# Kernel tuning notes

Measured on AMD Instinct MI355X. Metric: run time of the kernel, lower is better.

The kernel has to match this reference:

```python
import jax, jax.numpy as jnp
import numpy as np

B, TQ, TK = 4, 128, 512
DQ = DK = DV = H = 1024


def setup_inputs() -> dict:
    key = jax.random.key(0)
    ks = jax.random.split(key, 7)
    s = 0.05  # keep tanh out of saturation
    return {
        "query": jax.random.normal(ks[0], (B, TQ, DQ), dtype=jnp.float32),
        "key": jax.random.normal(ks[1], (B, TK, DK), dtype=jnp.float32),
        "value": jax.random.normal(ks[2], (B, TK, DV), dtype=jnp.float32),
        "Wq": jax.random.normal(ks[3], (DQ, H), dtype=jnp.float32) * s,
        "bq": jax.random.normal(ks[4], (H,), dtype=jnp.float32) * s,
        "Wk": jax.random.normal(ks[5], (DK, H), dtype=jnp.float32) * s,
        "v": jax.random.normal(ks[6], (H,), dtype=jnp.float32) * s,
    }


def reference(query, key, value, Wq, bq, Wk, v):
    # additive (Bahdanau) attention
    wq = jnp.einsum("bqd,dh->bqh", query, Wq) + bq      # [B,Tq,H]
    uh = jnp.einsum("bkd,dh->bkh", key, Wk)             # [B,Tk,H]
    # broadcast add -> [B,Tq,Tk,H], tanh, project to scalar score
    scores = jnp.einsum("bqkh,h->bqk",
                        jnp.tanh(wq[:, :, None, :] + uh[:, None, :, :]), v)
    attn = jax.nn.softmax(scores, axis=-1)              # [B,Tq,Tk]
    h = jnp.einsum("bqk,bkv->bqv", attn, value)         # [B,Tq,Dv]
    return h, attn
```

## Files before the change

### kernel.cpp

```cpp
#include <hip/hip_runtime.h>
#include <hip/hip_bf16.h>

typedef float f32x4 __attribute__((ext_vector_type(4)));
typedef float f32x2 __attribute__((ext_vector_type(2)));
typedef short s16x8 __attribute__((ext_vector_type(8)));
typedef short s16x4 __attribute__((ext_vector_type(4)));

#define NB  4
#define NTQ 128
#define NTK 512
#define NH  1024
#define ECLAMP 3.0e4f

__device__ __forceinline__ unsigned short f2bf(float x) {
    unsigned u = __builtin_bit_cast(unsigned, x);
    u += 0x7FFFu + ((u >> 16) & 1u);
    return (unsigned short)(u >> 16);
}

#define K2E  2.8853900817779268f

#define GLD16(gp, lp) __builtin_amdgcn_global_load_lds( \
    (const __attribute__((address_space(1))) unsigned int*)(gp), \
    (__attribute__((address_space(3))) unsigned int*)(lp), 16, 0, 0)

__global__ __launch_bounds__(256) void prep_kernel(
    const float* __restrict__ Q, const float* __restrict__ K,
    const float* __restrict__ Wq, const float* __restrict__ Wk,
    const float* __restrict__ value,
    short* __restrict__ Qb, short* __restrict__ Kb,
    short* __restrict__ WqT, short* __restrict__ WkT, short* __restrict__ valT)
{
    const int t = threadIdx.x, bx = blockIdx.x;
    if (bx < 640) {
        const float* src; short* dst; size_t base;
        if (bx < 128) { src = Q; dst = Qb; base = (size_t)bx * 4096; }
        else          { src = K; dst = Kb; base = (size_t)(bx - 128) * 4096; }
        #pragma unroll
        for (int i = 0; i < 4; ++i) {
            const size_t off = base + (size_t)(i * 256 + t) * 4;
            const float4 vv = *(const float4*)(src + off);
            s16x4 o = { (short)f2bf(vv.x), (short)f2bf(vv.y),
                        (short)f2bf(vv.z), (short)f2bf(vv.w) };
            *(s16x4*)(dst + off) = o;
        }
        return;
    }
    __shared__ float tile[64][65];
    const int i = bx - 640;
    const float* src; short* dst; int Cs, Rs, r0, c0;
    if (i < 256)      { src = Wq; dst = WqT; Cs = 1024; Rs = 1024; r0 = (i >> 4) * 64; c0 = (i & 15) * 64; }
    else if (i < 512) { const int j = i - 256; src = Wk; dst = WkT; Cs = 1024; Rs = 1024; r0 = (j >> 4) * 64; c0 = (j & 15) * 64; }
    else {
        const int j = i - 512, b = j >> 7, ti = j & 127;
        src = value + (size_t)b * 512 * 1024; dst = valT + (size_t)b * 1024 * 512;
        Cs = 1024; Rs = 512; r0 = (ti >> 4) * 64; c0 = (ti & 15) * 64;
    }
    {
        const int c = (t & 15) * 4;
        #pragma unroll
        for (int it = 0; it < 4; ++it) {
            const int r = (t >> 4) + it * 16;
            const float4 vv = *(const float4*)(src + (size_t)(r0 + r) * Cs + c0 + c);
            tile[r][c + 0] = vv.x; tile[r][c + 1] = vv.y;
            tile[r][c + 2] = vv.z; tile[r][c + 3] = vv.w;
        }
    }
    __syncthreads();
    {
        const int r = (t & 15) * 4;
        #pragma unroll
        for (int it = 0; it < 4; ++it) {
            const int c = (t >> 4) + it * 16;
            s16x4 o = { (short)f2bf(tile[r + 0][c]), (short)f2bf(tile[r + 1][c]),
                        (short)f2bf(tile[r + 2][c]), (short)f2bf(tile[r + 3][c]) };
            *(s16x4*)(dst + (size_t)(c0 + c) * Rs + r0 + r) = o;
        }
    }
}

__global__ __launch_bounds__(256) void mm_kernel(
    const short* __restrict__ Qb, const short* __restrict__ Kb,
    const short* __restrict__ WqT, const short* __restrict__ WkT,
    const float* __restrict__ bq,
    float* __restrict__ Ea_out, unsigned short* __restrict__ EbT)
{
    __shared__ short ldsA[2][128][64];
    __shared__ short ldsB[2][64][64];
    const int t = threadIdx.x;
    const int bx0 = blockIdx.x;
    const int bx = (bx0 & 7) * 40 + (bx0 >> 3);
    const bool g1 = bx < 64;
    const short *A, *B; int m0, n0;
    if (g1) { A = Qb; B = WqT; m0 = (bx >> 4) * 128; n0 = (bx & 15) * 64; }
    else    { const int i = bx - 64; A = Kb; B = WkT; m0 = (i >> 4) * 128; n0 = (i & 15) * 64; }
    A += (size_t)m0 * 1024; B += (size_t)n0 * 1024;

    f32x4 acc[4][2];
    #pragma unroll
    for (int i = 0; i < 4; ++i)
        #pragma unroll
        for (int j = 0; j < 2; ++j) acc[i][j] = f32x4{0.f, 0.f, 0.f, 0.f};

    const int lane = t & 63, wid = t >> 6;
    const int wr = wid >> 1, wc = wid & 1;
    const int fr = lane & 15, fko = (lane >> 4) * 16;

    #define STAGE_MM(buf, k0) do {                                              \
        _Pragma("unroll")                                                       \
        for (int it = 0; it < 4; ++it) {                                        \
            const int idx = it * 256 + t;                                       \
            const int row = idx >> 3, c16 = idx & 7;                            \
            const int sc = c16 ^ (row & 7);                                     \
            GLD16(A + (size_t)row * 1024 + (k0) + sc * 8,                       \
                  &ldsA[buf][0][0] + idx * 8);                                  \
        }                                                                       \
        _Pragma("unroll")                                                       \
        for (int it = 0; it < 2; ++it) {                                        \
            const int idx = it * 256 + t;                                       \
            const int row = idx >> 3, c16 = idx & 7;                            \
            const int sc = c16 ^ (row & 7);                                     \
            GLD16(B + (size_t)row * 1024 + (k0) + sc * 8,                       \
                  &ldsB[buf][0][0] + idx * 8);                                  \
        }                                                                       \
    } while (0)

    #define COMPUTE_MM(buf) do {                                                \
        _Pragma("unroll")                                                       \
        for (int kk = 0; kk < 2; ++kk) {                                        \
            s16x8 af[4], bfv[2];                                                \
            _Pragma("unroll")                                                   \
            for (int i = 0; i < 4; ++i) {                                       \
                const int rowA = wr * 64 + i * 16 + fr;                         \
                int offA = rowA * 128 + kk * 64 + fko; offA ^= (rowA & 7) << 4; \
                af[i] = *(const s16x8*)((const char*)&ldsA[buf][0][0] + offA);  \
            }                                                                   \
            _Pragma("unroll")                                                   \
            for (int ni = 0; ni < 2; ++ni) {                                    \
                const int rowB = wc * 32 + ni * 16 + fr;                        \
                int offB = rowB * 128 + kk * 64 + fko; offB ^= (rowB & 7) << 4; \
                bfv[ni] = *(const s16x8*)((const char*)&ldsB[buf][0][0] + offB);\
            }                                                                   \
            _Pragma("unroll")                                                   \
            for (int mi = 0; mi < 4; ++mi)                                      \
                _Pragma("unroll")                                               \
                for (int ni = 0; ni < 2; ++ni)                                  \
                    acc[mi][ni] = __builtin_amdgcn_mfma_f32_16x16x32_bf16(      \
                                      af[mi], bfv[ni], acc[mi][ni], 0, 0, 0);   \
        }                                                                       \
    } while (0)

    STAGE_MM(0, 0);
    __syncthreads();
    int cur = 0;
    for (int s = 0; s < 15; ++s) {
        STAGE_MM(cur ^ 1, (s + 1) * 64);
        COMPUTE_MM(cur);
        __syncthreads();
        cur ^= 1;
    }
    COMPUTE_MM(cur);

    const int row0 = (lane >> 4) * 4;
    if (g1) {
        #pragma unroll
        for (int ni = 0; ni < 2; ++ni) {
            const int n = n0 + wc * 32 + ni * 16 + fr;
            const float bias = bq[n];
            #pragma unroll
            for (int mi = 0; mi < 4; ++mi) {
                const int m = m0 + wr * 64 + mi * 16 + row0;
                #pragma unroll
                for (int j = 0; j < 4; ++j)
                    Ea_out[(size_t)(m + j) * 1024 + n] =
                        fminf(__builtin_amdgcn_exp2f(K2E * (acc[mi][ni][j] + bias)), ECLAMP);
            }
        }
    } else {
        #pragma unroll
        for (int mi = 0; mi < 4; ++mi) {
            const int m = m0 + wr * 64 + mi * 16 + row0;
            const int b = m >> 9, kk = m & 511;
            #pragma unroll
            for (int ni = 0; ni < 2; ++ni) {
                const int n = n0 + wc * 32 + ni * 16 + fr;
                s16x4 ev;
                #pragma unroll
                for (int j = 0; j < 4; ++j)
                    ev[j] = (short)f2bf(fminf(__builtin_amdgcn_exp2f(K2E * acc[mi][ni][j]), ECLAMP));
                *(s16x4*)&EbT[((size_t)b * 1024 + n) * 512 + kk] = ev;
            }
        }
    }
    #undef STAGE_MM
    #undef COMPUTE_MM
}

__global__ __launch_bounds__(1024, 8) void scores_z(
    const unsigned short* __restrict__ EbT, const float* __restrict__ Ea,
    const float* __restrict__ v, float* __restrict__ zout)
{
    __shared__ float4 s_eav[1024];
    __shared__ float  s_part[16][2][256];
    const int t = threadIdx.x, bx = blockIdx.x;
    const int combo = bx & 7;
    const int b  = combo >> 1, kh = combo & 1;
    const int q2 = bx >> 3;
    const int bq0 = b * 128 + q2 * 2;
    const int kq = t & 63;
    const int hs = t >> 6;

    s_eav[t] = make_float4(Ea[(size_t)(bq0 + 0) * 1024 + t],
                           Ea[(size_t)(bq0 + 1) * 1024 + t],
                           v[t], 0.f);
    __syncthreads();

    const int h0 = hs * 64;
    const uint2* up = (const uint2*)(EbT + ((size_t)(b * 1024 + h0)) * 512
                                     + kh * 256 + kq * 4);
    float a00 = 0.f, a01 = 0.f, a02 = 0.f, a03 = 0.f;
    float a10 = 0.f, a11 = 0.f, a12 = 0.f, a13 = 0.f;
    #pragma unroll 2
    for (int hg = 0; hg < 16; ++hg) {
        const int hb = hg * 4;
        const uint2 r0 = up[(size_t)(hb + 0) * 128];
        const uint2 r1 = up[(size_t)(hb + 1) * 128];
        const uint2 r2 = up[(size_t)(hb + 2) * 128];
        const uint2 r3 = up[(size_t)(hb + 3) * 128];
        const float4 ev0 = s_eav[h0 + hb + 0];
        const float4 ev1 = s_eav[h0 + hb + 1];
        const float4 ev2 = s_eav[h0 + hb + 2];
        const float4 ev3 = s_eav[h0 + hb + 3];
        float eb0[4], eb1[4], eb2[4], eb3[4];
        eb0[0] = __builtin_bit_cast(float, r0.x << 16);
        eb0[1] = __builtin_bit_cast(float, r0.x & 0xFFFF0000u);
        eb0[2] = __builtin_bit_cast(float, r0.y << 16);
        eb0[3] = __builtin_bit_cast(float, r0.y & 0xFFFF0000u);
        eb1[0] = __builtin_bit_cast(float, r1.x << 16);
        eb1[1] = __builtin_bit_cast(float, r1.x & 0xFFFF0000u);
        eb1[2] = __builtin_bit_cast(float, r1.y << 16);
        eb1[3] = __builtin_bit_cast(float, r1.y & 0xFFFF0000u);
        eb2[0] = __builtin_bit_cast(float, r2.x << 16);
        eb2[1] = __builtin_bit_cast(float, r2.x & 0xFFFF0000u);
        eb2[2] = __builtin_bit_cast(float, r2.y << 16);
        eb2[3] = __builtin_bit_cast(float, r2.y & 0xFFFF0000u);
        eb3[0] = __builtin_bit_cast(float, r3.x << 16);
        eb3[1] = __builtin_bit_cast(float, r3.x & 0xFFFF0000u);
        eb3[2] = __builtin_bit_cast(float, r3.y << 16);
        eb3[3] = __builtin_bit_cast(float, r3.y & 0xFFFF0000u);

        #define GRP4(accv, ea0, ea1, ea2, ea3, kk) do {                         \
            const float u0 = __builtin_fmaf(ea0, eb0[kk], 1.0f);                \
            const float u1 = __builtin_fmaf(ea1, eb1[kk], 1.0f);                \
            const float u2 = __builtin_fmaf(ea2, eb2[kk], 1.0f);                \
            const float u3 = __builtin_fmaf(ea3, eb3[kk], 1.0f);                \
            const float d01 = u0 * u1, d23 = u2 * u3;                           \
            float n01 = ev0.z * u1; n01 = __builtin_fmaf(ev1.z, u0, n01);       \
            float n23 = ev2.z * u3; n23 = __builtin_fmaf(ev3.z, u2, n23);       \
            float n = n01 * d23; n = __builtin_fmaf(n23, d01, n);               \
            const float r = __builtin_amdgcn_rcpf(d01 * d23);                   \
            accv = __builtin_fmaf(n, r, accv);                                  \
        } while (0)

        GRP4(a00, ev0.x, ev1.x, ev2.x, ev3.x, 0);
        GRP4(a01, ev0.x, ev1.x, ev2.x, ev3.x, 1);
        GRP4(a02, ev0.x, ev1.x, ev2.x, ev3.x, 2);
        GRP4(a03, ev0.x, ev1.x, ev2.x, ev3.x, 3);
        GRP4(a10, ev0.y, ev1.y, ev2.y, ev3.y, 0);
        GRP4(a11, ev0.y, ev1.y, ev2.y, ev3.y, 1);
        GRP4(a12, ev0.y, ev1.y, ev2.y, ev3.y, 2);
        GRP4(a13, ev0.y, ev1.y, ev2.y, ev3.y, 3);
        #undef GRP4
    }
    *(f32x4*)&s_part[hs][0][kq * 4] = f32x4{a00, a01, a02, a03};
    *(f32x4*)&s_part[hs][1][kq * 4] = f32x4{a10, a11, a12, a13};
    __syncthreads();

    if (t < 512) {
        const int kk = t & 255, qq = t >> 8;
        float z = 0.f;
        #pragma unroll
        for (int j = 0; j < 16; ++j) z += s_part[j][qq][kk];
        zout[(size_t)(bq0 + qq) * 512 + kh * 256 + kk] = -2.0f * z;
    }
}

__global__ __launch_bounds__(512) void softmax_kernel(
    const float* __restrict__ zin, float* __restrict__ attn_out,
    short* __restrict__ attnb)
{
    __shared__ float s_red[16];
    const int t = threadIdx.x, bqi = blockIdx.x;
    const float z = zin[(size_t)bqi * 512 + t];
    const int lane = t & 63, wid = t >> 6;

    float m = z;
    #pragma unroll
    for (int off = 32; off > 0; off >>= 1)
        m = fmaxf(m, __shfl_xor(m, off, 64));
    if (lane == 0) s_red[wid] = m;
    __syncthreads();
    float mx = s_red[0];
    #pragma unroll
    for (int w = 1; w < 8; ++w) mx = fmaxf(mx, s_red[w]);
    const float p = __expf(z - mx);
    __syncthreads();

    float sl = p;
    #pragma unroll
    for (int off = 32; off > 0; off >>= 1)
        sl += __shfl_xor(sl, off, 64);
    if (lane == 0) s_red[wid] = sl;
    __syncthreads();
    float s = 0.f;
    #pragma unroll
    for (int w = 0; w < 8; ++w) s += s_red[w];

    const float a = p * (1.0f / s);
    attn_out[(size_t)bqi * 512 + t] = a;
    attnb[(size_t)bqi * 512 + t] = (short)f2bf(a);
}

__global__ __launch_bounds__(256) void pv_gemm(
    const short* __restrict__ attnb, const short* __restrict__ valT,
    float* __restrict__ outh)
{
    __shared__ short ldsA[2][128][64];
    __shared__ short ldsB[2][64][64];
    const int t = threadIdx.x, bx = blockIdx.x;
    const int b = bx >> 4, nt = bx & 15;
    const int n0 = nt * 64;
    const short* A = attnb + (size_t)b * 128 * 512;
    const short* B = valT + (size_t)b * 1024 * 512 + (size_t)n0 * 512;

    f32x4 acc[4][2];
    #pragma unroll
    for (int i = 0; i < 4; ++i)
        #pragma unroll
        for (int j = 0; j < 2; ++j) acc[i][j] = f32x4{0.f, 0.f, 0.f, 0.f};

    const int lane = t & 63, wid = t >> 6;
    const int wr = wid >> 1, wc = wid & 1;
    const int fr = lane & 15, fko = (lane >> 4) * 16;

    #define STAGE_PV(buf, k0) do {                                              \
        _Pragma("unroll")                                                       \
        for (int it = 0; it < 4; ++it) {                                        \
            const int idx = it * 256 + t;                                       \
            const int row = idx >> 3, c16 = idx & 7;                            \
            const int sc = c16 ^ (row & 7);                                     \
            GLD16(A + (size_t)row * 512 + (k0) + sc * 8,                        \
                  &ldsA[buf][0][0] + idx * 8);                                  \
        }                                                                       \
        _Pragma("unroll")                                                       \
        for (int it = 0; it < 2; ++it) {                                        \
            const int idx = it * 256 + t;                                       \
            const int row = idx >> 3, c16 = idx & 7;                            \
            const int sc = c16 ^ (row & 7);                                     \
            GLD16(B + (size_t)row * 512 + (k0) + sc * 8,                        \
                  &ldsB[buf][0][0] + idx * 8);                                  \
        }                                                                       \
    } while (0)

    #define COMPUTE_PV(buf) do {                                                \
        _Pragma("unroll")                                                       \
        for (int kk = 0; kk < 2; ++kk) {                                        \
            s16x8 af[4], bfv[2];                                                \
            _Pragma("unroll")                                                   \
            for (int i = 0; i < 4; ++i) {                                       \
                const int rowA = wr * 64 + i * 16 + fr;                         \
                int offA = rowA * 128 + kk * 64 + fko; offA ^= (rowA & 7) << 4; \
                af[i] = *(const s16x8*)((const char*)&ldsA[buf][0][0] + offA);  \
            }                                                                   \
            _Pragma("unroll")                                                   \
            for (int ni = 0; ni < 2; ++ni) {                                    \
                const int rowB = wc * 32 + ni * 16 + fr;                        \
                int offB = rowB * 128 + kk * 64 + fko; offB ^= (rowB & 7) << 4; \
                bfv[ni] = *(const s16x8*)((const char*)&ldsB[buf][0][0] + offB);\
            }                                                                   \
            _Pragma("unroll")                                                   \
            for (int mi = 0; mi < 4; ++mi)                                      \
                _Pragma("unroll")                                               \
                for (int ni = 0; ni < 2; ++ni)                                  \
                    acc[mi][ni] = __builtin_amdgcn_mfma_f32_16x16x32_bf16(      \
                                      af[mi], bfv[ni], acc[mi][ni], 0, 0, 0);   \
        }                                                                       \
    } while (0)

    STAGE_PV(0, 0);
    __syncthreads();
    int cur = 0;
    for (int s = 0; s < 7; ++s) {
        STAGE_PV(cur ^ 1, (s + 1) * 64);
        COMPUTE_PV(cur);
        __syncthreads();
        cur ^= 1;
    }
    COMPUTE_PV(cur);

    const int row0 = (lane >> 4) * 4;
    #pragma unroll
    for (int ni = 0; ni < 2; ++ni) {
        const int n = n0 + wc * 32 + ni * 16 + fr;
        #pragma unroll
        for (int mi = 0; mi < 4; ++mi) {
            const int m = wr * 64 + mi * 16 + row0;
            #pragma unroll
            for (int j = 0; j < 4; ++j)
                outh[(size_t)(b * 128 + m + j) * 1024 + n] = acc[mi][ni][j];
        }
    }
    #undef STAGE_PV
    #undef COMPUTE_PV
}

extern "C" void kernel_launch(void* const* d_in, const int* in_sizes, int n_in,
                              void* d_out, int out_size, void* d_ws, size_t ws_size,
                              hipStream_t stream)
{
    const float* query = (const float*)d_in[0];
    const float* key   = (const float*)d_in[1];
    const float* value = (const float*)d_in[2];
    const float* Wq    = (const float*)d_in[3];
    const float* bq    = (const float*)d_in[4];
    const float* Wk    = (const float*)d_in[5];
    const float* v     = (const float*)d_in[6];
    float* out = (float*)d_out;

    char* w = (char*)d_ws;
    float*          ws_Ea  = (float*)w;
    unsigned short* ws_EbT = (unsigned short*)(w + (2u << 20));
    short* Qb     = (short*)(w + (6u << 20));
    short* Kb     = (short*)(w + (7u << 20));
    short* WqT    = (short*)(w + (11u << 20));
    short* WkT    = (short*)(w + (13u << 20));
    short* valT   = (short*)(w + (15u << 20));
    short* attnb  = (short*)(w + (19u << 20));
    float* zbuf   = (float*)(w + (20u << 20));

    float* out_h    = out;
    float* out_attn = out + (size_t)NB * NTQ * NH;

    prep_kernel   <<<dim3(1664), dim3(256),  0, stream>>>(query, key, Wq, Wk, value,
                                                          Qb, Kb, WqT, WkT, valT);
    mm_kernel     <<<dim3(320),  dim3(256),  0, stream>>>(Qb, Kb, WqT, WkT, bq, ws_Ea, ws_EbT);
    scores_z      <<<dim3(512),  dim3(1024), 0, stream>>>(ws_EbT, ws_Ea, v, zbuf);
    softmax_kernel<<<dim3(512),  dim3(512),  0, stream>>>(zbuf, out_attn, attnb);
    pv_gemm       <<<dim3(64),   dim3(256),  0, stream>>>(attnb, valT, out_h);
}
```

Measured before the change: 66.76 us.

## Fuse score reduction with softmax into one kernel covering full key range

```diff
diff --git a/kernel.cpp b/kernel.cpp
--- a/kernel.cpp
+++ b/kernel.cpp
@@ -196,32 +196,33 @@
     #undef COMPUTE_MM
 }
 
-__global__ __launch_bounds__(1024, 8) void scores_z(
+__global__ __launch_bounds__(1024, 4) void scores_softmax(
     const unsigned short* __restrict__ EbT, const float* __restrict__ Ea,
-    const float* __restrict__ v, float* __restrict__ zout)
+    const float* __restrict__ v,
+    float* __restrict__ attn_out, short* __restrict__ attnb)
 {
     __shared__ float4 s_eav[1024];
-    __shared__ float  s_part[16][2][256];
+    __shared__ float  s_part[8][2][512];
+    __shared__ float  s_red[16];
     const int t = threadIdx.x, bx = blockIdx.x;
-    const int combo = bx & 7;
-    const int b  = combo >> 1, kh = combo & 1;
-    const int q2 = bx >> 3;
+    const int b = bx & 3;
+    const int q2 = bx >> 2;
     const int bq0 = b * 128 + q2 * 2;
-    const int kq = t & 63;
-    const int hs = t >> 6;
+    const int kq = t & 127;
+    const int hs = t >> 7;
+    const int lane = t & 63, wid = t >> 6;
 
     s_eav[t] = make_float4(Ea[(size_t)(bq0 + 0) * 1024 + t],
                            Ea[(size_t)(bq0 + 1) * 1024 + t],
                            v[t], 0.f);
     __syncthreads();
 
-    const int h0 = hs * 64;
-    const uint2* up = (const uint2*)(EbT + ((size_t)(b * 1024 + h0)) * 512
-                                     + kh * 256 + kq * 4);
+    const int h0 = hs * 128;
+    const uint2* up = (const uint2*)(EbT + ((size_t)(b * 1024 + h0)) * 512) + kq;
     float a00 = 0.f, a01 = 0.f, a02 = 0.f, a03 = 0.f;
     float a10 = 0.f, a11 = 0.f, a12 = 0.f, a13 = 0.f;
     #pragma unroll 2
-    for (int hg = 0; hg < 16; ++hg) {
+    for (int hg = 0; hg < 32; ++hg) {
         const int hb = hg * 4;
         const uint2 r0 = up[(size_t)(hb + 0) * 128];
         const uint2 r1 = up[(size_t)(hb + 1) * 128];
@@ -276,23 +277,11 @@
     *(f32x4*)&s_part[hs][1][kq * 4] = f32x4{a10, a11, a12, a13};
     __syncthreads();
 
-    if (t < 512) {
-        const int kk = t & 255, qq = t >> 8;
-        float z = 0.f;
-        #pragma unroll
-        for (int j = 0; j < 16; ++j) z += s_part[j][qq][kk];
-        zout[(size_t)(bq0 + qq) * 512 + kh * 256 + kk] = -2.0f * z;
-    }
-}
-
-__global__ __launch_bounds__(512) void softmax_kernel(
-    const float* __restrict__ zin, float* __restrict__ attn_out,
-    short* __restrict__ attnb)
-{
-    __shared__ float s_red[16];
-    const int t = threadIdx.x, bqi = blockIdx.x;
-    const float z = zin[(size_t)bqi * 512 + t];
-    const int lane = t & 63, wid = t >> 6;
+    const int kk = t & 511, qq = t >> 9;
+    float z = 0.f;
+    #pragma unroll
+    for (int j = 0; j < 8; ++j) z += s_part[j][qq][kk];
+    z *= -2.0f;
 
     float m = z;
     #pragma unroll
@@ -300,9 +289,9 @@
         m = fmaxf(m, __shfl_xor(m, off, 64));
     if (lane == 0) s_red[wid] = m;
     __syncthreads();
-    float mx = s_red[0];
-    #pragma unroll
-    for (int w = 1; w < 8; ++w) mx = fmaxf(mx, s_red[w]);
+    float mx = s_red[qq * 8];
+    #pragma unroll
+    for (int w = 1; w < 8; ++w) mx = fmaxf(mx, s_red[qq * 8 + w]);
     const float p = __expf(z - mx);
     __syncthreads();
 
@@ -314,11 +303,11 @@
     __syncthreads();
     float s = 0.f;
     #pragma unroll
-    for (int w = 0; w < 8; ++w) s += s_red[w];
+    for (int w = 0; w < 8; ++w) s += s_red[qq * 8 + w];
 
     const float a = p * (1.0f / s);
-    attn_out[(size_t)bqi * 512 + t] = a;
-    attnb[(size_t)bqi * 512 + t] = (short)f2bf(a);
+    attn_out[(size_t)(bq0 + qq) * 512 + kk] = a;
+    attnb[(size_t)(bq0 + qq) * 512 + kk] = (short)f2bf(a);
 }
 
 __global__ __launch_bounds__(256) void pv_gemm(
@@ -436,7 +425,6 @@
     short* WkT    = (short*)(w + (13u << 20));
     short* valT   = (short*)(w + (15u << 20));
     short* attnb  = (short*)(w + (19u << 20));
-    float* zbuf   = (float*)(w + (20u << 20));
 
     float* out_h    = out;
     float* out_attn = out + (size_t)NB * NTQ * NH;
@@ -444,7 +432,6 @@
     prep_kernel   <<<dim3(1664), dim3(256),  0, stream>>>(query, key, Wq, Wk, value,
                                                           Qb, Kb, WqT, WkT, valT);
     mm_kernel     <<<dim3(320),  dim3(256),  0, stream>>>(Qb, Kb, WqT, WkT, bq, ws_Ea, ws_EbT);
-    scores_z      <<<dim3(512),  dim3(1024), 0, stream>>>(ws_EbT, ws_Ea, v, zbuf);
-    softmax_kernel<<<dim3(512),  dim3(512),  0, stream>>>(zbuf, out_attn, attnb);
+    scores_softmax<<<dim3(256),  dim3(1024), 0, stream>>>(ws_EbT, ws_Ea, v, out_attn, attnb);
     pv_gemm       <<<dim3(64),   dim3(256),  0, stream>>>(attnb, valT, out_h);
 }
```

After: 65.92 us. No clear change (-1.3%).
